# Kernel optimization log

Hardware: AMD Instinct MI355X
Metric: run time of the kernel (lower is better)

The kernel has to match this reference:

```python
import jax, jax.numpy as jnp
import numpy as np

B, N, DIM = 2, 4096, 1024
DEPTH, HEADS, DHEAD = 6, 8, 128
BUCKET = 64          # blindspot_size -> causal_linear_attn bucket_size
DFF = 4 * DIM
EPS_LN = 1e-5
EPS_ATTN = 1e-3


def setup_inputs() -> dict:
    key = jax.random.key(0)
    ks = jax.random.split(key, 16)
    s = 0.02
    HD = HEADS * DHEAD
    inp = {
        "x":     jax.random.normal(ks[0], (B, N, DIM), jnp.float32),
        "ln1_g": jnp.ones((DEPTH, DIM), jnp.float32),
        "ln1_b": jnp.zeros((DEPTH, DIM), jnp.float32),
        "Wq":    jax.random.normal(ks[1], (DEPTH, DIM, HD), jnp.float32) * s,
        "Wk":    jax.random.normal(ks[2], (DEPTH, DIM, HD), jnp.float32) * s,
        "Wv":    jax.random.normal(ks[3], (DEPTH, DIM, HD), jnp.float32) * s,
        "Wo":    jax.random.normal(ks[4], (DEPTH, HD, DIM), jnp.float32) * s,
        "bo":    jnp.zeros((DEPTH, DIM), jnp.float32),
        "ln2_g": jnp.ones((DEPTH, DIM), jnp.float32),
        "ln2_b": jnp.zeros((DEPTH, DIM), jnp.float32),
        "W1":    jax.random.normal(ks[5], (DEPTH, DIM, DFF), jnp.float32) * s,
        "b1":    jnp.zeros((DEPTH, DFF), jnp.float32),
        "W2":    jax.random.normal(ks[6], (DEPTH, DFF, DIM), jnp.float32) * s,
        "b2":    jnp.zeros((DEPTH, DIM), jnp.float32),
    }
    return inp


def layernorm(x, g, b):
    m = jnp.mean(x, axis=-1, keepdims=True)
    v = jnp.var(x, axis=-1, keepdims=True)
    return (x - m) * jax.lax.rsqrt(v + EPS_LN) * g + b


def causal_linear_attn(q, k, v, bucket_size=BUCKET, eps=EPS_ATTN):
    # q,k,v: [b, h, n, e]; n divisible by bucket_size. Blindspot bucketed causal linear attn.
    b, h, n, e = q.shape
    q = jax.nn.softmax(q, axis=-1) * (e ** -0.5)
    k = jnp.exp(k)
    u = n // bucket_size
    bq = q.reshape(b, h, u, bucket_size, e)
    bk = k.reshape(b, h, u, bucket_size, e)
    bv = v.reshape(b, h, u, bucket_size, e)
    b_k_cumsum = jnp.cumsum(bk.sum(axis=-2), axis=2)                     # [b,h,u,e]
    context = jnp.cumsum(jnp.einsum('bhund,bhune->bhude', bk, bv), axis=2)  # [b,h,u,e,e]
    if bucket_size > 1:
        # shift by one bucket: each bucket only sees strictly earlier buckets (blindspot)
        context = jnp.pad(context, ((0, 0), (0, 0), (1, 0), (0, 0), (0, 0)))[:, :, :-1]
        b_k_cumsum = jnp.pad(b_k_cumsum, ((0, 0), (0, 0), (1, 0), (0, 0)))[:, :, :-1]
    D_inv = 1.0 / jnp.maximum(jnp.einsum('bhud,bhund->bhun', b_k_cumsum, bq), eps)
    out = jnp.einsum('bhund,bhude,bhun->bhune', bq, context, D_inv)
    return out.reshape(b, h, n, e)


def _forward(x, ln1_g, ln1_b, Wq, Wk, Wv, Wo, bo, ln2_g, ln2_b, W1, b1, W2, b2):
    def split_heads(t):  # [b,n,h*e] -> [b,h,n,e]
        return t.reshape(B, N, HEADS, DHEAD).transpose(0, 2, 1, 3)

    def layer(x, p):
        g1, bb1_, wq, wk, wv, wo, bo_, g2, bb2_, w1, bias1, w2, bias2 = p
        h = layernorm(x, g1, bb1_)
        q, k, v = split_heads(h @ wq), split_heads(h @ wk), split_heads(h @ wv)
        a = causal_linear_attn(q, k, v)
        a = a.transpose(0, 2, 1, 3).reshape(B, N, HEADS * DHEAD)
        x = x + a @ wo + bo_
        h = layernorm(x, g2, bb2_)
        x = x + jax.nn.gelu(h @ w1 + bias1, approximate=False) @ w2 + bias2
        return x, None

    params = (ln1_g, ln1_b, Wq, Wk, Wv, Wo, bo, ln2_g, ln2_b, W1, b1, W2, b2)
    x, _ = jax.lax.scan(layer, x, params)
    return x


def reference(x, ln1_g, ln1_b, Wq, Wk, Wv, Wo, bo, ln2_g, ln2_b, W1, b1, W2, b2):
    return _forward(x, ln1_g, ln1_b, Wq, Wk, Wv, Wo, bo, ln2_g, ln2_b, W1, b1, W2, b2)
```

## Files before the change

### kernel.cpp

```cpp
#include <hip/hip_runtime.h>
#include <hip/hip_bf16.h>
#include <stdint.h>

#define TOK 8192
#define DIM 1024
#define NSEQ 4096
#define NH 8
#define DHD 128
#define NU 64
#define DFF 4096
#define NBH 16
#define QKVN 3072

typedef unsigned short u16;
typedef unsigned int u32;
typedef short bf16x8 __attribute__((ext_vector_type(8)));
typedef float f32x4 __attribute__((ext_vector_type(4)));

__device__ __forceinline__ float bu2f(u16 u) { return __uint_as_float(((u32)u) << 16); }
__device__ __forceinline__ u16 f2bu(float f) {
  union { __hip_bfloat16 b; u16 u; } cv; cv.b = __float2bfloat16(f); return cv.u;
}

typedef __attribute__((address_space(1))) void gvoid_t;
typedef __attribute__((address_space(3))) void lvoid_t;
__device__ __forceinline__ void gload16(void* lds, const void* g) {
#if __has_builtin(__builtin_amdgcn_global_load_lds)
  __builtin_amdgcn_global_load_lds((const gvoid_t*)g, (lvoid_t*)lds, 16, 0, 0);
#else
  const int l = threadIdx.x & 63;
  ((uint4*)lds)[l] = *(const uint4*)g;
#endif
}

__global__ __launch_bounds__(256) void wtrans_kernel(const float* __restrict__ W,
    u16* __restrict__ Wt, int K, int N, int dStride, int rowOff)
{
  __shared__ float T[32][33];
  const int tid = threadIdx.x;
  const size_t soff = (size_t)blockIdx.z * K * N;
  const size_t doff = (size_t)blockIdx.z * dStride;
  const int n0 = blockIdx.x << 5, k0 = blockIdx.y << 5;
  const int r = tid >> 3, c4 = (tid & 7) << 2;
  float4 v = *(const float4*)(W + soff + (size_t)(k0 + r) * N + n0 + c4);
  T[r][c4] = v.x; T[r][c4 + 1] = v.y; T[r][c4 + 2] = v.z; T[r][c4 + 3] = v.w;
  __syncthreads();
  u32 lo = (u32)f2bu(T[c4][r]) | ((u32)f2bu(T[c4 + 1][r]) << 16);
  u32 hi = (u32)f2bu(T[c4 + 2][r]) | ((u32)f2bu(T[c4 + 3][r]) << 16);
  *(uint2*)(Wt + doff + (size_t)(rowOff + n0 + r) * K + k0 + c4) = make_uint2(lo, hi);
}

__global__ __launch_bounds__(256) void ln_kernel(const float* __restrict__ x,
    const float* __restrict__ g, const float* __restrict__ bt, u16* __restrict__ h)
{
  const int row = blockIdx.x, tid = threadIdx.x;
  const int w = tid >> 6, l = tid & 63;
  float4 v = ((const float4*)(x + (size_t)row * DIM))[tid];
  float s = v.x + v.y + v.z + v.w;
  float s2 = v.x * v.x + v.y * v.y + v.z * v.z + v.w * v.w;
#pragma unroll
  for (int off = 32; off; off >>= 1) { s += __shfl_down(s, off); s2 += __shfl_down(s2, off); }
  __shared__ float ps[8];
  __shared__ float mv[2];
  if (l == 0) { ps[w] = s; ps[4 + w] = s2; }
  __syncthreads();
  if (tid == 0) {
    float S = ps[0] + ps[1] + ps[2] + ps[3];
    float S2 = ps[4] + ps[5] + ps[6] + ps[7];
    float mean = S * (1.f / 1024.f);
    float var = S2 * (1.f / 1024.f) - mean * mean;
    mv[0] = mean; mv[1] = rsqrtf(var + 1e-5f);
  }
  __syncthreads();
  const float mean = mv[0], inv = mv[1];
  const int c = tid * 4;
  float o0 = (v.x - mean) * inv * g[c + 0] + bt[c + 0];
  float o1 = (v.y - mean) * inv * g[c + 1] + bt[c + 1];
  float o2 = (v.z - mean) * inv * g[c + 2] + bt[c + 2];
  float o3 = (v.w - mean) * inv * g[c + 3] + bt[c + 3];
  u32 lo = (u32)f2bu(o0) | ((u32)f2bu(o1) << 16);
  u32 hi = (u32)f2bu(o2) | ((u32)f2bu(o3) << 16);
  ((uint2*)(h + (size_t)row * DIM))[tid] = make_uint2(lo, hi);
}

template<int EPI>
__global__ __launch_bounds__(256, 2) void gemm_kernel(
    const u16* __restrict__ A, const u16* __restrict__ Bt, void* Cout,
    const float* __restrict__ bias, const float* res, int M, int N, int K)
{
  __shared__ __align__(16) u16 As[2][128 * 32];
  __shared__ __align__(16) u16 Bs[2][128 * 32];
  const int tid = threadIdx.x;
  const int w = tid >> 6, l = tid & 63;
  const int gx = gridDim.x;
  const int nwg = gx * gridDim.y;
  const int orig = blockIdx.y * gx + blockIdx.x;
  const int qq = nwg >> 3, rr = nwg & 7, xcd = orig & 7, lin = orig >> 3;
  const int wg = (xcd < rr ? xcd * (qq + 1) : rr * (qq + 1) + (xcd - rr) * qq) + lin;
  const int brow = (wg / gx) << 7, bcol = (wg % gx) << 7;
  const int wr = (w >> 1) << 6, wc = (w & 1) << 6;
  const int lr = l & 15, lk = (l >> 4) << 3;
  f32x4 acc[4][4] = {};
  const int nk = K >> 5;

#define STAGE_G(buf, kt)                                                        \
  {                                                                             \
    _Pragma("unroll")                                                           \
    for (int j = 0; j < 2; ++j) {                                               \
      int c = j * 256 + tid;                                                    \
      int rrow = c >> 2, k8 = (c & 3) << 3;                                     \
      int ub = (j * 256 + w * 64) * 8;                                          \
      gload16(&As[buf][ub], A + (size_t)(brow + rrow) * K + (kt) * 32 + k8);    \
      gload16(&Bs[buf][ub], Bt + (size_t)(bcol + rrow) * K + (kt) * 32 + k8);   \
    }                                                                           \
  }

  STAGE_G(0, 0);
  __syncthreads();
  for (int kt = 0; kt < nk; ++kt) {
    int buf = kt & 1;
    if (kt + 1 < nk) STAGE_G(buf ^ 1, kt + 1);
    bf16x8 a[4], bb[4];
#pragma unroll
    for (int m = 0; m < 4; ++m) a[m] = *(const bf16x8*)&As[buf][(wr + m * 16 + lr) * 32 + lk];
#pragma unroll
    for (int n = 0; n < 4; ++n) bb[n] = *(const bf16x8*)&Bs[buf][(wc + n * 16 + lr) * 32 + lk];
#pragma unroll
    for (int m = 0; m < 4; ++m)
#pragma unroll
      for (int n = 0; n < 4; ++n)
        acc[m][n] = __builtin_amdgcn_mfma_f32_16x16x32_bf16(a[m], bb[n], acc[m][n], 0, 0, 0);
    __syncthreads();
  }
#undef STAGE_G
  const int l4 = (l >> 4) << 2;
#pragma unroll
  for (int m = 0; m < 4; ++m) {
#pragma unroll
    for (int n = 0; n < 4; ++n) {
      int col = bcol + wc + n * 16 + lr;
#pragma unroll
      for (int r = 0; r < 4; ++r) {
        int row = brow + wr + m * 16 + l4 + r;
        size_t idx = (size_t)row * N + col;
        float v0 = acc[m][n][r];
        if (EPI == 0) {
          ((u16*)Cout)[idx] = f2bu(v0);
        } else if (EPI == 1) {
          ((float*)Cout)[idx] = v0 + bias[col] + res[idx];
        } else {
          float t = v0 + bias[col];
          ((u16*)Cout)[idx] = f2bu(0.5f * t * (1.0f + erff(t * 0.70710678118654752f)));
        }
      }
    }
  }
}

__global__ __launch_bounds__(256) void qsoftmax_kernel(const u16* __restrict__ qkv, u16* __restrict__ qs)
{
  const int w = threadIdx.x >> 6, l = threadIdx.x & 63;
  const size_t gid = (size_t)blockIdx.x * 4 + w;
  const size_t tok = gid >> 3;
  const int h = (int)(gid & 7);
  const u16* row = qkv + tok * QKVN + h * 128;
  u16* orow = qs + tok * DIM + h * 128;
  u32 p = *(const u32*)(row + l * 2);
  float f0 = bu2f((u16)(p & 0xffff)), f1 = bu2f((u16)(p >> 16));
  float m = fmaxf(f0, f1);
#pragma unroll
  for (int off = 32; off; off >>= 1) m = fmaxf(m, __shfl_xor(m, off));
  float e0 = expf(f0 - m), e1 = expf(f1 - m);
  float s = e0 + e1;
#pragma unroll
  for (int off = 32; off; off >>= 1) s += __shfl_xor(s, off);
  float sc = 0.08838834764831845f / s;
  u32 o = (u32)f2bu(e0 * sc) | ((u32)f2bu(e1 * sc) << 16);
  *(u32*)(orow + l * 2) = o;
}

__global__ __launch_bounds__(256) void kvt_kernel(
    const u16* __restrict__ kin, const u16* __restrict__ vin,
    u16* __restrict__ ket, u16* __restrict__ vt)
{
  __shared__ u16 T[128 * 72];
  const int tid = threadIdx.x;
  const int t64 = blockIdx.x, bh = blockIdx.y;
  const int b = bh >> 3, h = bh & 7;
  for (int pass = 0; pass < 2; ++pass) {
    const u16* src = pass ? vin : kin;
    u16* dst = pass ? vt : ket;
    if (pass) __syncthreads();
#pragma unroll
    for (int j = 0; j < 4; ++j) {
      int c = j * 256 + tid;
      int i = c >> 4, e8 = (c & 15) << 3;
      bf16x8 dv = *(const bf16x8*)(src + ((size_t)(b * NSEQ + t64 * 64 + i)) * QKVN + h * 128 + e8);
#pragma unroll
      for (int jj = 0; jj < 8; ++jj) {
        float f = bu2f((u16)dv[jj]);
        if (pass == 0) f = expf(f);
        T[(e8 + jj) * 72 + i] = f2bu(f);
      }
    }
    __syncthreads();
#pragma unroll
    for (int j = 0; j < 4; ++j) {
      int c = j * 256 + tid;
      int e = c >> 3, n8 = (c & 7) << 3;
      bf16x8 o;
#pragma unroll
      for (int jj = 0; jj < 8; ++jj) o[jj] = (short)T[e * 72 + n8 + jj];
      *(bf16x8*)(dst + ((size_t)(bh * 128 + e)) * NSEQ + t64 * 64 + n8) = o;
    }
  }
}

__global__ void ksum_kernel(const u16* __restrict__ ket, float* __restrict__ Ksum)
{
  const int u = blockIdx.x, bh = blockIdx.y, e = threadIdx.x;
  const u16* p = ket + ((size_t)(bh * 128 + e)) * NSEQ + u * 64;
  float s = 0.f;
#pragma unroll
  for (int i = 0; i < 64; ++i) s += bu2f(p[i]);
  Ksum[(((size_t)bh * 64 + u) << 7) + e] = s;
}

__global__ void kc_kernel(const float* __restrict__ Ksum, float* __restrict__ Kc)
{
  const int bh = blockIdx.x, e = threadIdx.x;
  float run = 0.f;
  for (int u = 0; u < 64; ++u) {
    size_t i = (((size_t)bh * 64 + u) << 7) + e;
    Kc[i] = run;
    run += Ksum[i];
  }
}

__global__ __launch_bounds__(256, 2) void ctx_kernel(
    const u16* __restrict__ vt, const u16* __restrict__ ket, u16* __restrict__ ctxT)
{
  __shared__ __align__(16) u16 Av[128 * 64];
  __shared__ __align__(16) u16 Bk[128 * 64];
  const int tid = threadIdx.x, w = tid >> 6, l = tid & 63;
  const int u = blockIdx.x, bh = blockIdx.y;
  const int lr = l & 15, lk = (l >> 4) << 3;
#pragma unroll
  for (int j = 0; j < 4; ++j) {
    int c = j * 256 + tid;
    int row = c >> 3, i8 = (c & 7) << 3;
    size_t goff = ((size_t)(bh * 128 + row)) * NSEQ + u * 64 + i8;
    int ub = (j * 256 + w * 64) * 8;
    gload16(&Av[ub], vt + goff);
    gload16(&Bk[ub], ket + goff);
  }
  __syncthreads();
  const int wr = (w >> 1) << 6, wc = (w & 1) << 6;
  f32x4 acc[4][4] = {};
#pragma unroll
  for (int ks = 0; ks < 2; ++ks) {
    bf16x8 a[4], bb[4];
#pragma unroll
    for (int m = 0; m < 4; ++m) a[m] = *(const bf16x8*)&Av[(wr + m * 16 + lr) * 64 + ks * 32 + lk];
#pragma unroll
    for (int n = 0; n < 4; ++n) bb[n] = *(const bf16x8*)&Bk[(wc + n * 16 + lr) * 64 + ks * 32 + lk];
#pragma unroll
    for (int m = 0; m < 4; ++m)
#pragma unroll
      for (int n = 0; n < 4; ++n)
        acc[m][n] = __builtin_amdgcn_mfma_f32_16x16x32_bf16(a[m], bb[n], acc[m][n], 0, 0, 0);
  }
  u16* out = ctxT + ((size_t)(bh * 64 + u) << 14);
  const int l4 = (l >> 4) << 2;
#pragma unroll
  for (int m = 0; m < 4; ++m)
#pragma unroll
    for (int n = 0; n < 4; ++n)
#pragma unroll
      for (int r = 0; r < 4; ++r) {
        int e = wr + m * 16 + l4 + r, d = wc + n * 16 + lr;
        out[e * 128 + d] = f2bu(acc[m][n][r]);
      }
}

__global__ void cumsum_kernel(const u16* __restrict__ ctxT, u16* __restrict__ ctxc)
{
  const size_t base = ((size_t)blockIdx.y << 20) + (size_t)blockIdx.x * 256 + threadIdx.x;
  const u16* src = ctxT + base;
  u16* dst = ctxc + base;
  float run = 0.f;
  for (int u = 0; u < 64; ++u) {
    u16 cvv = src[(size_t)u << 14];
    dst[(size_t)u << 14] = f2bu(run);
    run += bu2f(cvv);
  }
}

__global__ __launch_bounds__(256, 2) void attnout_kernel(
    const u16* __restrict__ qs, const u16* __restrict__ ctxc,
    const float* __restrict__ Kc, u16* __restrict__ aout)
{
  __shared__ __align__(16) u16 Aq[64 * 128];
  __shared__ __align__(16) u16 Bc[128 * 128];
  __shared__ float KcS[128];
  __shared__ float Dinv[64];
  const int tid = threadIdx.x, w = tid >> 6, l = tid & 63;
  const int u = blockIdx.x, bh = blockIdx.y;
  const int b = bh >> 3, h = bh & 7;
  const int lr = l & 15, lk = (l >> 4) << 3;
#pragma unroll
  for (int j = 0; j < 4; ++j) {
    int c = j * 256 + tid;
    int n = c >> 4, d8 = (c & 15) << 3;
    gload16(&Aq[(j * 256 + w * 64) * 8],
            qs + ((size_t)(b * NSEQ + u * 64 + n)) * DIM + h * 128 + d8);
  }
  const u16* csrc = ctxc + ((size_t)(bh * 64 + u) << 14);
#pragma unroll
  for (int j = 0; j < 8; ++j) {
    int c = j * 256 + tid;
    gload16(&Bc[(j * 256 + w * 64) * 8], csrc + (size_t)c * 8);
  }
  if (tid < 128) KcS[tid] = Kc[(((size_t)bh * 64 + u) << 7) + tid];
  __syncthreads();
  if (tid < 64) {
    float s = 0.f;
#pragma unroll
    for (int dd = 0; dd < 128; ++dd) {
      int d = (dd + tid * 2) & 127;
      s += bu2f(Aq[tid * 128 + d]) * KcS[d];
    }
    Dinv[tid] = 1.f / fmaxf(s, 1e-3f);
  }
  __syncthreads();
  f32x4 acc[4][2] = {};
#pragma unroll
  for (int ks = 0; ks < 4; ++ks) {
    bf16x8 a[4], bb[2];
#pragma unroll
    for (int m = 0; m < 4; ++m) a[m] = *(const bf16x8*)&Aq[(m * 16 + lr) * 128 + ks * 32 + lk];
#pragma unroll
    for (int n = 0; n < 2; ++n) bb[n] = *(const bf16x8*)&Bc[(w * 32 + n * 16 + lr) * 128 + ks * 32 + lk];
#pragma unroll
    for (int m = 0; m < 4; ++m)
#pragma unroll
      for (int n = 0; n < 2; ++n)
        acc[m][n] = __builtin_amdgcn_mfma_f32_16x16x32_bf16(a[m], bb[n], acc[m][n], 0, 0, 0);
  }
  const int l4 = (l >> 4) << 2;
#pragma unroll
  for (int m = 0; m < 4; ++m)
#pragma unroll
    for (int n = 0; n < 2; ++n)
#pragma unroll
      for (int r = 0; r < 4; ++r) {
        int nrow = m * 16 + l4 + r;
        int e = w * 32 + n * 16 + lr;
        float v = acc[m][n][r] * Dinv[nrow];
        aout[((size_t)(b * NSEQ + u * 64 + nrow)) * DIM + h * 128 + e] = f2bu(v);
      }
}

extern "C" void kernel_launch(void* const* d_in, const int* in_sizes, int n_in,
                              void* d_out, int out_size, void* d_ws, size_t ws_size,
                              hipStream_t stream)
{
  (void)in_sizes; (void)n_in; (void)out_size; (void)ws_size;
  const float* x_in = (const float*)d_in[0];
  const float* ln1g = (const float*)d_in[1];
  const float* ln1b = (const float*)d_in[2];
  const float* Wq   = (const float*)d_in[3];
  const float* Wk   = (const float*)d_in[4];
  const float* Wv   = (const float*)d_in[5];
  const float* Wo   = (const float*)d_in[6];
  const float* bo   = (const float*)d_in[7];
  const float* ln2g = (const float*)d_in[8];
  const float* ln2b = (const float*)d_in[9];
  const float* W1   = (const float*)d_in[10];
  const float* b1   = (const float*)d_in[11];
  const float* W2   = (const float*)d_in[12];
  const float* b2   = (const float*)d_in[13];
  float* x = (float*)d_out;

  char* ws = (char*)d_ws;
  size_t off = 0;
  auto alloc = [&](size_t bytes) -> char* {
    char* p = ws + off;
    off += (bytes + 255) & ~(size_t)255;
    return p;
  };
  const size_t SW = (size_t)6 * 1024 * 1024;
  const size_t BW = (size_t)6 * 4096 * 1024;
  u16* Wqkvt = (u16*)alloc(SW * 3 * 2);
  u16* Wot = (u16*)alloc(SW * 2);
  u16* W1t = (u16*)alloc(BW * 2);
  u16* W2t = (u16*)alloc(BW * 2);
  u16* hbuf = (u16*)alloc((size_t)TOK * DIM * 2);
  u16* qsb  = (u16*)alloc((size_t)TOK * DIM * 2);
  u16* ket  = (u16*)alloc((size_t)TOK * DIM * 2);
  u16* vtb  = (u16*)alloc((size_t)TOK * DIM * 2);
  u16* ab   = (u16*)alloc((size_t)TOK * DIM * 2);
  float* Ksum = (float*)alloc((size_t)NBH * 64 * 128 * 4);
  float* Kc   = (float*)alloc((size_t)NBH * 64 * 128 * 4);
  char* R = alloc((size_t)TOK * DFF * 2);
  u16* qkvb = (u16*)R;
  u16* ctxT = (u16*)R;
  u16* ctxc = (u16*)(R + ((size_t)NBH * 64 * 128 * 128) * 2);
  u16* mid  = (u16*)R;

  wtrans_kernel<<<dim3(32, 32, 6), 256, 0, stream>>>(Wq, Wqkvt, 1024, 1024, QKVN * 1024, 0);
  wtrans_kernel<<<dim3(32, 32, 6), 256, 0, stream>>>(Wk, Wqkvt, 1024, 1024, QKVN * 1024, 1024);
  wtrans_kernel<<<dim3(32, 32, 6), 256, 0, stream>>>(Wv, Wqkvt, 1024, 1024, QKVN * 1024, 2048);
  wtrans_kernel<<<dim3(32, 32, 6), 256, 0, stream>>>(Wo, Wot, 1024, 1024, 1024 * 1024, 0);
  wtrans_kernel<<<dim3(128, 32, 6), 256, 0, stream>>>(W1, W1t, 1024, 4096, 4096 * 1024, 0);
  wtrans_kernel<<<dim3(32, 128, 6), 256, 0, stream>>>(W2, W2t, 4096, 1024, 4096 * 1024, 0);
  hipMemcpyAsync(x, x_in, (size_t)TOK * DIM * 4, hipMemcpyDeviceToDevice, stream);

  for (int d = 0; d < 6; ++d) {
    ln_kernel<<<TOK, 256, 0, stream>>>(x, ln1g + d * DIM, ln1b + d * DIM, hbuf);
    gemm_kernel<0><<<dim3(24, 64), 256, 0, stream>>>(hbuf, Wqkvt + (size_t)d * QKVN * 1024, qkvb, nullptr, nullptr, TOK, QKVN, DIM);
    qsoftmax_kernel<<<TOK * NH / 4, 256, 0, stream>>>(qkvb, qsb);
    kvt_kernel<<<dim3(64, NBH), 256, 0, stream>>>(qkvb + 1024, qkvb + 2048, ket, vtb);
    ksum_kernel<<<dim3(64, NBH), 128, 0, stream>>>(ket, Ksum);
    kc_kernel<<<NBH, 128, 0, stream>>>(Ksum, Kc);
    ctx_kernel<<<dim3(64, NBH), 256, 0, stream>>>(vtb, ket, ctxT);
    cumsum_kernel<<<dim3(64, NBH), 256, 0, stream>>>(ctxT, ctxc);
    attnout_kernel<<<dim3(64, NBH), 256, 0, stream>>>(qsb, ctxc, Kc, ab);
    gemm_kernel<1><<<dim3(8, 64), 256, 0, stream>>>(ab, Wot + (size_t)d * 1024 * 1024, x, bo + d * DIM, x, TOK, DIM, DIM);
    ln_kernel<<<TOK, 256, 0, stream>>>(x, ln2g + d * DIM, ln2b + d * DIM, hbuf);
    gemm_kernel<2><<<dim3(32, 64), 256, 0, stream>>>(hbuf, W1t + (size_t)d * DFF * 1024, mid, b1 + d * DFF, nullptr, TOK, DFF, DIM);
    gemm_kernel<1><<<dim3(8, 64), 256, 0, stream>>>(mid, W2t + (size_t)d * DFF * 1024, x, b2 + d * DIM, x, TOK, DIM, DFF);
  }
}
```

Before: 2.649 ms.

## Add 256x256 eight-wave pipelined GEMM for the QKV and FFN-up projections

Adds a new bf16 MFMA GEMM kernel with 256x256 output tiles, 512 threads, a K-step of 64 and XOR-swizzled LDS. It splits each K-step into four phases that interleave global-to-LDS staging with MFMA quadrants, using barriers and raised wave priority around the MFMA blocks. The QKV projection and the W1+GELU projection now use this kernel. The older 128x128 kernel is reduced to the residual epilogue only, for the Wo and W2 GEMMs. The larger tiles give more data reuse per LDS load, but they need about 128KB of LDS per block, which limits occupancy, and they produce fewer workgroups, so wave quantization across CUs could suffer.

Result: slower. 3.061 ms (+15.6%).

```diff
diff --git a/kernel.cpp b/kernel.cpp
--- a/kernel.cpp
+++ b/kernel.cpp
@@ -84,6 +84,115 @@
 }
 
 template<int EPI>
+__global__ __launch_bounds__(512, 2) void gemm8_kernel(
+    const u16* __restrict__ A, const u16* __restrict__ Bt, void* Cout,
+    const float* __restrict__ bias, int M, int N, int K)
+{
+  __shared__ __align__(16) u16 As[2][2][8192];
+  __shared__ __align__(16) u16 Bs[2][2][8192];
+  const int tid = threadIdx.x;
+  const int w = tid >> 6, l = tid & 63;
+  const int wm = w >> 2, wn = w & 3;
+  const int lr = l & 15, lk = (l >> 4) << 3;
+  const int gx = gridDim.x;
+  const int nwg = gx * gridDim.y;
+  const int orig = blockIdx.y * gx + blockIdx.x;
+  const int qq = nwg >> 3, rr = nwg & 7, xcd = orig & 7, lin = orig >> 3;
+  const int wg = (xcd < rr ? xcd * (qq + 1) : rr * (qq + 1) + (xcd - rr) * qq) + lin;
+  const int brow = (wg / gx) << 8, bcol = (wg % gx) << 8;
+  const int nk = K >> 6;
+  const int srow = w * 8 + (l >> 3);
+  const int scol = ((l & 7) * 8) ^ ((l & 32) ? 16 : 0);
+  const int swz = ((l >> 2) & 1) << 4;
+  const int colK0 = lk ^ swz, colK1 = (32 + lk) ^ swz;
+
+  f32x4 acc[8][4] = {};
+  bf16x8 af[4][2];
+  bf16x8 bf[2][2][2];
+
+#define STAGE_A8(b_, h_, kt_) { _Pragma("unroll") for (int c = 0; c < 2; ++c)   \
+    gload16(&As[b_][h_][c * 4096 + w * 512],                                    \
+      A + (size_t)(brow + (h_) * 128 + c * 64 + srow) * K + (kt_) * 64 + scol); }
+#define STAGE_B8(b_, h_, kt_) { _Pragma("unroll") for (int c = 0; c < 2; ++c)   \
+    gload16(&Bs[b_][h_][c * 4096 + w * 512],                                    \
+      Bt + (size_t)(bcol + (h_) * 128 + c * 64 + srow) * K + (kt_) * 64 + scol); }
+#define LOAD_AF(b_, mh_) { _Pragma("unroll") for (int m = 0; m < 4; ++m) {      \
+    const u16* p_ = &As[b_][wm][((mh_) * 64 + m * 16 + lr) * 64];               \
+    af[m][0] = *(const bf16x8*)(p_ + colK0);                                    \
+    af[m][1] = *(const bf16x8*)(p_ + colK1); } }
+#define LOAD_BF(b_, nh_) { _Pragma("unroll") for (int n = 0; n < 2; ++n) {      \
+    const u16* p_ = &Bs[b_][wn >> 1][((wn & 1) * 64 + (nh_) * 32 + n * 16 + lr) * 64]; \
+    bf[nh_][n][0] = *(const bf16x8*)(p_ + colK0);                               \
+    bf[nh_][n][1] = *(const bf16x8*)(p_ + colK1); } }
+#define MFMA_Q(mh_, nh_) { __builtin_amdgcn_s_setprio(1);                       \
+    _Pragma("unroll") for (int m = 0; m < 4; ++m)                               \
+    _Pragma("unroll") for (int n = 0; n < 2; ++n) {                             \
+      acc[(mh_)*4+m][(nh_)*2+n] = __builtin_amdgcn_mfma_f32_16x16x32_bf16(      \
+          af[m][0], bf[nh_][n][0], acc[(mh_)*4+m][(nh_)*2+n], 0, 0, 0);         \
+      acc[(mh_)*4+m][(nh_)*2+n] = __builtin_amdgcn_mfma_f32_16x16x32_bf16(      \
+          af[m][1], bf[nh_][n][1], acc[(mh_)*4+m][(nh_)*2+n], 0, 0, 0); }       \
+    __builtin_amdgcn_s_setprio(0); }
+#define PHASE_BAR() { __builtin_amdgcn_sched_barrier(0);                        \
+    __builtin_amdgcn_s_barrier(); __builtin_amdgcn_sched_barrier(0); }
+
+  STAGE_A8(0, 0, 0); STAGE_A8(0, 1, 0);
+  STAGE_B8(0, 0, 0); STAGE_B8(0, 1, 0);
+  STAGE_B8(1, 0, 1); STAGE_B8(1, 1, 1);
+  asm volatile("s_waitcnt vmcnt(4)" ::: "memory");
+  PHASE_BAR();
+
+  for (int t = 0; t < nk; ++t) {
+    const int buf = t & 1, nb = buf ^ 1;
+    LOAD_AF(buf, 0); LOAD_BF(buf, 0);
+    if (t + 1 < nk) STAGE_A8(nb, 0, t + 1);
+    PHASE_BAR();
+    MFMA_Q(0, 0);
+    PHASE_BAR();
+    LOAD_BF(buf, 1);
+    if (t + 1 < nk) STAGE_A8(nb, 1, t + 1);
+    PHASE_BAR();
+    MFMA_Q(0, 1);
+    PHASE_BAR();
+    LOAD_AF(buf, 1);
+    if (t + 2 < nk) STAGE_B8(buf, 0, t + 2);
+    PHASE_BAR();
+    MFMA_Q(1, 0);
+    PHASE_BAR();
+    if (t + 2 < nk) STAGE_B8(buf, 1, t + 2);
+    PHASE_BAR();
+    MFMA_Q(1, 1);
+    asm volatile("s_waitcnt vmcnt(4)" ::: "memory");
+    PHASE_BAR();
+  }
+#undef STAGE_A8
+#undef STAGE_B8
+#undef LOAD_AF
+#undef LOAD_BF
+#undef MFMA_Q
+#undef PHASE_BAR
+
+  const int l4 = (l >> 4) << 2;
+#pragma unroll
+  for (int mi = 0; mi < 8; ++mi) {
+#pragma unroll
+    for (int nj = 0; nj < 4; ++nj) {
+      int col = bcol + wn * 64 + nj * 16 + lr;
+#pragma unroll
+      for (int r = 0; r < 4; ++r) {
+        int row = brow + wm * 128 + mi * 16 + l4 + r;
+        size_t idx = (size_t)row * N + col;
+        float v0 = acc[mi][nj][r];
+        if (EPI == 0) {
+          ((u16*)Cout)[idx] = f2bu(v0);
+        } else {
+          float tt = v0 + bias[col];
+          ((u16*)Cout)[idx] = f2bu(0.5f * tt * (1.0f + erff(tt * 0.70710678118654752f)));
+        }
+      }
+    }
+  }
+}
+
 __global__ __launch_bounds__(256, 2) void gemm_kernel(
     const u16* __restrict__ A, const u16* __restrict__ Bt, void* Cout,
     const float* __restrict__ bias, const float* res, int M, int N, int K)
@@ -143,15 +252,7 @@
       for (int r = 0; r < 4; ++r) {
         int row = brow + wr + m * 16 + l4 + r;
         size_t idx = (size_t)row * N + col;
-        float v0 = acc[m][n][r];
-        if (EPI == 0) {
-          ((u16*)Cout)[idx] = f2bu(v0);
-        } else if (EPI == 1) {
-          ((float*)Cout)[idx] = v0 + bias[col] + res[idx];
-        } else {
-          float t = v0 + bias[col];
-          ((u16*)Cout)[idx] = f2bu(0.5f * t * (1.0f + erff(t * 0.70710678118654752f)));
-        }
+        ((float*)Cout)[idx] = acc[m][n][r] + bias[col] + res[idx];
       }
     }
   }
@@ -418,7 +519,7 @@
 
   for (int d = 0; d < 6; ++d) {
     ln_kernel<<<TOK, 256, 0, stream>>>(x, ln1g + d * DIM, ln1b + d * DIM, hbuf);
-    gemm_kernel<0><<<dim3(24, 64), 256, 0, stream>>>(hbuf, Wqkvt + (size_t)d * QKVN * 1024, qkvb, nullptr, nullptr, TOK, QKVN, DIM);
+    gemm8_kernel<0><<<dim3(12, 32), 512, 0, stream>>>(hbuf, Wqkvt + (size_t)d * QKVN * 1024, qkvb, nullptr, TOK, QKVN, DIM);
     qsoftmax_kernel<<<TOK * NH / 4, 256, 0, stream>>>(qkvb, qsb);
     kvt_kernel<<<dim3(64, NBH), 256, 0, stream>>>(qkvb + 1024, qkvb + 2048, ket, vtb);
     ksum_kernel<<<dim3(64, NBH), 128, 0, stream>>>(ket, Ksum);
@@ -426,9 +527,9 @@
     ctx_kernel<<<dim3(64, NBH), 256, 0, stream>>>(vtb, ket, ctxT);
     cumsum_kernel<<<dim3(64, NBH), 256, 0, stream>>>(ctxT, ctxc);
     attnout_kernel<<<dim3(64, NBH), 256, 0, stream>>>(qsb, ctxc, Kc, ab);
-    gemm_kernel<1><<<dim3(8, 64), 256, 0, stream>>>(ab, Wot + (size_t)d * 1024 * 1024, x, bo + d * DIM, x, TOK, DIM, DIM);
+    gemm_kernel<<<dim3(8, 64), 256, 0, stream>>>(ab, Wot + (size_t)d * 1024 * 1024, x, bo + d * DIM, x, TOK, DIM, DIM);
     ln_kernel<<<TOK, 256, 0, stream>>>(x, ln2g + d * DIM, ln2b + d * DIM, hbuf);
-    gemm_kernel<2><<<dim3(32, 64), 256, 0, stream>>>(hbuf, W1t + (size_t)d * DFF * 1024, mid, b1 + d * DFF, nullptr, TOK, DFF, DIM);
-    gemm_kernel<1><<<dim3(8, 64), 256, 0, stream>>>(mid, W2t + (size_t)d * DFF * 1024, x, b2 + d * DIM, x, TOK, DIM, DFF);
-  }
-}
+    gemm8_kernel<2><<<dim3(16, 32), 512, 0, stream>>>(hbuf, W1t + (size_t)d * DFF * 1024, mid, b1 + d * DFF, TOK, DFF, DIM);
+    gemm_kernel<<<dim3(8, 64), 256, 0, stream>>>(mid, W2t + (size_t)d * DFF * 1024, x, b2 + d * DIM, x, TOK, DIM, DFF);
+  }
+}
```

## Enlarge GEMM tiles to 256x128 and fold key-sum into kvt transpose kernel

Applied to the files above, without the earlier changes.

The GEMM kernel's M tile grows from 128 to 256 rows. Each wave now computes a 128x64 sub-tile with 8x4 MFMA accumulators, and each A fragment is loaded per m-iteration and reused across the 4 B fragments. All GEMM grids are halved in y to match. Separately, the per-bucket key sum is computed from the shared-memory transpose tile inside kvt_kernel, which removes the ksum_kernel launch and its re-read of ket. The larger tile doubles accumulator registers and A shared memory, which can lower occupancy under launch_bounds(256,2) and halves the block count.

Result: slower. 3.494 ms (+31.9%).

```diff
diff --git a/kernel.cpp b/kernel.cpp
--- a/kernel.cpp
+++ b/kernel.cpp
@@ -88,7 +88,7 @@
     const u16* __restrict__ A, const u16* __restrict__ Bt, void* Cout,
     const float* __restrict__ bias, const float* res, int M, int N, int K)
 {
-  __shared__ __align__(16) u16 As[2][128 * 32];
+  __shared__ __align__(16) u16 As[2][256 * 32];
   __shared__ __align__(16) u16 Bs[2][128 * 32];
   const int tid = threadIdx.x;
   const int w = tid >> 6, l = tid & 63;
@@ -97,21 +97,27 @@
   const int orig = blockIdx.y * gx + blockIdx.x;
   const int qq = nwg >> 3, rr = nwg & 7, xcd = orig & 7, lin = orig >> 3;
   const int wg = (xcd < rr ? xcd * (qq + 1) : rr * (qq + 1) + (xcd - rr) * qq) + lin;
-  const int brow = (wg / gx) << 7, bcol = (wg % gx) << 7;
-  const int wr = (w >> 1) << 6, wc = (w & 1) << 6;
+  const int brow = (wg / gx) << 8, bcol = (wg % gx) << 7;
+  const int wr = (w >> 1) << 7, wc = (w & 1) << 6;
   const int lr = l & 15, lk = (l >> 4) << 3;
-  f32x4 acc[4][4] = {};
+  f32x4 acc[8][4] = {};
   const int nk = K >> 5;
 
 #define STAGE_G(buf, kt)                                                        \
   {                                                                             \
+    _Pragma("unroll")                                                           \
+    for (int j = 0; j < 4; ++j) {                                               \
+      int c = j * 256 + tid;                                                    \
+      int rrow = c >> 2, k8 = (c & 3) << 3;                                     \
+      gload16(&As[buf][(j * 256 + w * 64) * 8],                                 \
+              A + (size_t)(brow + rrow) * K + (kt) * 32 + k8);                  \
+    }                                                                           \
     _Pragma("unroll")                                                           \
     for (int j = 0; j < 2; ++j) {                                               \
       int c = j * 256 + tid;                                                    \
       int rrow = c >> 2, k8 = (c & 3) << 3;                                     \
-      int ub = (j * 256 + w * 64) * 8;                                          \
-      gload16(&As[buf][ub], A + (size_t)(brow + rrow) * K + (kt) * 32 + k8);    \
-      gload16(&Bs[buf][ub], Bt + (size_t)(bcol + rrow) * K + (kt) * 32 + k8);   \
+      gload16(&Bs[buf][(j * 256 + w * 64) * 8],                                 \
+              Bt + (size_t)(bcol + rrow) * K + (kt) * 32 + k8);                 \
     }                                                                           \
   }
 
@@ -120,22 +126,22 @@
   for (int kt = 0; kt < nk; ++kt) {
     int buf = kt & 1;
     if (kt + 1 < nk) STAGE_G(buf ^ 1, kt + 1);
-    bf16x8 a[4], bb[4];
-#pragma unroll
-    for (int m = 0; m < 4; ++m) a[m] = *(const bf16x8*)&As[buf][(wr + m * 16 + lr) * 32 + lk];
-#pragma unroll
-    for (int n = 0; n < 4; ++n) bb[n] = *(const bf16x8*)&Bs[buf][(wc + n * 16 + lr) * 32 + lk];
-#pragma unroll
-    for (int m = 0; m < 4; ++m)
+    bf16x8 b[4];
+#pragma unroll
+    for (int n = 0; n < 4; ++n) b[n] = *(const bf16x8*)&Bs[buf][(wc + n * 16 + lr) * 32 + lk];
+#pragma unroll
+    for (int m = 0; m < 8; ++m) {
+      bf16x8 a = *(const bf16x8*)&As[buf][(wr + m * 16 + lr) * 32 + lk];
 #pragma unroll
       for (int n = 0; n < 4; ++n)
-        acc[m][n] = __builtin_amdgcn_mfma_f32_16x16x32_bf16(a[m], bb[n], acc[m][n], 0, 0, 0);
+        acc[m][n] = __builtin_amdgcn_mfma_f32_16x16x32_bf16(a, b[n], acc[m][n], 0, 0, 0);
+    }
     __syncthreads();
   }
 #undef STAGE_G
   const int l4 = (l >> 4) << 2;
 #pragma unroll
-  for (int m = 0; m < 4; ++m) {
+  for (int m = 0; m < 8; ++m) {
 #pragma unroll
     for (int n = 0; n < 4; ++n) {
       int col = bcol + wc + n * 16 + lr;
@@ -181,7 +187,7 @@
 
 __global__ __launch_bounds__(256) void kvt_kernel(
     const u16* __restrict__ kin, const u16* __restrict__ vin,
-    u16* __restrict__ ket, u16* __restrict__ vt)
+    u16* __restrict__ ket, u16* __restrict__ vt, float* __restrict__ Ksum)
 {
   __shared__ u16 T[128 * 72];
   const int tid = threadIdx.x;
@@ -204,6 +210,12 @@
       }
     }
     __syncthreads();
+    if (pass == 0 && tid < 128) {
+      float s = 0.f;
+#pragma unroll
+      for (int i2 = 0; i2 < 64; ++i2) s += bu2f(T[tid * 72 + i2]);
+      Ksum[(((size_t)bh * 64 + t64) << 7) + tid] = s;
+    }
 #pragma unroll
     for (int j = 0; j < 4; ++j) {
       int c = j * 256 + tid;
@@ -214,16 +226,6 @@
       *(bf16x8*)(dst + ((size_t)(bh * 128 + e)) * NSEQ + t64 * 64 + n8) = o;
     }
   }
-}
-
-__global__ void ksum_kernel(const u16* __restrict__ ket, float* __restrict__ Ksum)
-{
-  const int u = blockIdx.x, bh = blockIdx.y, e = threadIdx.x;
-  const u16* p = ket + ((size_t)(bh * 128 + e)) * NSEQ + u * 64;
-  float s = 0.f;
-#pragma unroll
-  for (int i = 0; i < 64; ++i) s += bu2f(p[i]);
-  Ksum[(((size_t)bh * 64 + u) << 7) + e] = s;
 }
 
 __global__ void kc_kernel(const float* __restrict__ Ksum, float* __restrict__ Kc)
@@ -414,21 +416,20 @@
   wtrans_kernel<<<dim3(32, 32, 6), 256, 0, stream>>>(Wo, Wot, 1024, 1024, 1024 * 1024, 0);
   wtrans_kernel<<<dim3(128, 32, 6), 256, 0, stream>>>(W1, W1t, 1024, 4096, 4096 * 1024, 0);
   wtrans_kernel<<<dim3(32, 128, 6), 256, 0, stream>>>(W2, W2t, 4096, 1024, 4096 * 1024, 0);
-  hipMemcpyAsync(x, x_in, (size_t)TOK * DIM * 4, hipMemcpyDeviceToDevice, stream);
+  (void)hipMemcpyAsync(x, x_in, (size_t)TOK * DIM * 4, hipMemcpyDeviceToDevice, stream);
 
   for (int d = 0; d < 6; ++d) {
     ln_kernel<<<TOK, 256, 0, stream>>>(x, ln1g + d * DIM, ln1b + d * DIM, hbuf);
-    gemm_kernel<0><<<dim3(24, 64), 256, 0, stream>>>(hbuf, Wqkvt + (size_t)d * QKVN * 1024, qkvb, nullptr, nullptr, TOK, QKVN, DIM);
+    gemm_kernel<0><<<dim3(24, 32), 256, 0, stream>>>(hbuf, Wqkvt + (size_t)d * QKVN * 1024, qkvb, nullptr, nullptr, TOK, QKVN, DIM);
     qsoftmax_kernel<<<TOK * NH / 4, 256, 0, stream>>>(qkvb, qsb);
-    kvt_kernel<<<dim3(64, NBH), 256, 0, stream>>>(qkvb + 1024, qkvb + 2048, ket, vtb);
-    ksum_kernel<<<dim3(64, NBH), 128, 0, stream>>>(ket, Ksum);
+    kvt_kernel<<<dim3(64, NBH), 256, 0, stream>>>(qkvb + 1024, qkvb + 2048, ket, vtb, Ksum);
     kc_kernel<<<NBH, 128, 0, stream>>>(Ksum, Kc);
     ctx_kernel<<<dim3(64, NBH), 256, 0, stream>>>(vtb, ket, ctxT);
     cumsum_kernel<<<dim3(64, NBH), 256, 0, stream>>>(ctxT, ctxc);
     attnout_kernel<<<dim3(64, NBH), 256, 0, stream>>>(qsb, ctxc, Kc, ab);
-    gemm_kernel<1><<<dim3(8, 64), 256, 0, stream>>>(ab, Wot + (size_t)d * 1024 * 1024, x, bo + d * DIM, x, TOK, DIM, DIM);
+    gemm_kernel<1><<<dim3(8, 32), 256, 0, stream>>>(ab, Wot + (size_t)d * 1024 * 1024, x, bo + d * DIM, x, TOK, DIM, DIM);
     ln_kernel<<<TOK, 256, 0, stream>>>(x, ln2g + d * DIM, ln2b + d * DIM, hbuf);
-    gemm_kernel<2><<<dim3(32, 64), 256, 0, stream>>>(hbuf, W1t + (size_t)d * DFF * 1024, mid, b1 + d * DFF, nullptr, TOK, DFF, DIM);
-    gemm_kernel<1><<<dim3(8, 64), 256, 0, stream>>>(mid, W2t + (size_t)d * DFF * 1024, x, b2 + d * DIM, x, TOK, DIM, DFF);
-  }
-}
+    gemm_kernel<2><<<dim3(32, 32), 256, 0, stream>>>(hbuf, W1t + (size_t)d * DFF * 1024, mid, b1 + d * DFF, nullptr, TOK, DFF, DIM);
+    gemm_kernel<1><<<dim3(8, 32), 256, 0, stream>>>(mid, W2t + (size_t)d * DFF * 1024, x, b2 + d * DIM, x, TOK, DIM, DFF);
+  }
+}
```

## Fuse Q softmax into QKV GEMM epilogue, K-sum into kvt, use tanh GELU

Applied to the files above, without the earlier changes.

Adds a GEMM epilogue that computes the per-head softmax of Q directly from accumulators, using shared-memory cross-wave max/sum reductions, and writes the scaled result, removing the separate qsoftmax kernel. K column sums per bucket are computed inside kvt_kernel from the shared transpose tile, removing ksum_kernel. The erf GELU is replaced by a tanh approximation computed via exp, which changes numerics slightly relative to the exact GELU reference.

Measured after the change: 2.505 ms. 5.4% less time.

```diff
diff --git a/kernel.cpp b/kernel.cpp
--- a/kernel.cpp
+++ b/kernel.cpp
@@ -86,10 +86,12 @@
 template<int EPI>
 __global__ __launch_bounds__(256, 2) void gemm_kernel(
     const u16* __restrict__ A, const u16* __restrict__ Bt, void* Cout,
-    const float* __restrict__ bias, const float* res, int M, int N, int K)
+    const float* __restrict__ bias, const float* res, u16* __restrict__ qs,
+    int M, int N, int K)
 {
   __shared__ __align__(16) u16 As[2][128 * 32];
   __shared__ __align__(16) u16 Bs[2][128 * 32];
+  __shared__ float sm[2][128];
   const int tid = threadIdx.x;
   const int w = tid >> 6, l = tid & 63;
   const int gx = gridDim.x;
@@ -134,6 +136,69 @@
   }
 #undef STAGE_G
   const int l4 = (l >> 4) << 2;
+
+  if (EPI == 3 && bcol < 1024) {
+    const int wcol = w & 1;
+    float rmax[4][4], rsum[4][4];
+#pragma unroll
+    for (int m = 0; m < 4; ++m)
+#pragma unroll
+      for (int r = 0; r < 4; ++r) {
+        float v = fmaxf(fmaxf(acc[m][0][r], acc[m][1][r]), fmaxf(acc[m][2][r], acc[m][3][r]));
+#pragma unroll
+        for (int msk = 1; msk < 16; msk <<= 1) v = fmaxf(v, __shfl_xor(v, msk));
+        rmax[m][r] = v;
+      }
+    __syncthreads();
+#pragma unroll
+    for (int m = 0; m < 4; ++m)
+#pragma unroll
+      for (int r = 0; r < 4; ++r) sm[wcol][wr + m * 16 + l4 + r] = rmax[m][r];
+    __syncthreads();
+#pragma unroll
+    for (int m = 0; m < 4; ++m)
+#pragma unroll
+      for (int r = 0; r < 4; ++r) rmax[m][r] = fmaxf(rmax[m][r], sm[wcol ^ 1][wr + m * 16 + l4 + r]);
+#pragma unroll
+    for (int m = 0; m < 4; ++m)
+#pragma unroll
+      for (int r = 0; r < 4; ++r) {
+        float s = 0.f;
+#pragma unroll
+        for (int n = 0; n < 4; ++n) {
+          float e = __expf(acc[m][n][r] - rmax[m][r]);
+          acc[m][n][r] = e;
+          s += e;
+        }
+#pragma unroll
+        for (int msk = 1; msk < 16; msk <<= 1) s += __shfl_xor(s, msk);
+        rsum[m][r] = s;
+      }
+    __syncthreads();
+#pragma unroll
+    for (int m = 0; m < 4; ++m)
+#pragma unroll
+      for (int r = 0; r < 4; ++r) sm[wcol][wr + m * 16 + l4 + r] = rsum[m][r];
+    __syncthreads();
+#pragma unroll
+    for (int m = 0; m < 4; ++m)
+#pragma unroll
+      for (int r = 0; r < 4; ++r) rsum[m][r] += sm[wcol ^ 1][wr + m * 16 + l4 + r];
+#pragma unroll
+    for (int m = 0; m < 4; ++m)
+#pragma unroll
+      for (int n = 0; n < 4; ++n) {
+        int col = bcol + wc + n * 16 + lr;
+#pragma unroll
+        for (int r = 0; r < 4; ++r) {
+          int row = brow + wr + m * 16 + l4 + r;
+          float v = acc[m][n][r] * (0.08838834764831845f / rsum[m][r]);
+          qs[(size_t)row * DIM + col] = f2bu(v);
+        }
+      }
+    return;
+  }
+
 #pragma unroll
   for (int m = 0; m < 4; ++m) {
 #pragma unroll
@@ -144,44 +209,25 @@
         int row = brow + wr + m * 16 + l4 + r;
         size_t idx = (size_t)row * N + col;
         float v0 = acc[m][n][r];
-        if (EPI == 0) {
+        if (EPI == 0 || EPI == 3) {
           ((u16*)Cout)[idx] = f2bu(v0);
         } else if (EPI == 1) {
           ((float*)Cout)[idx] = v0 + bias[col] + res[idx];
         } else {
           float t = v0 + bias[col];
-          ((u16*)Cout)[idx] = f2bu(0.5f * t * (1.0f + erff(t * 0.70710678118654752f)));
+          float z = 1.5957691216057308f * (t + 0.044715f * t * t * t);
+          float e = __expf(z);
+          float th = (e - 1.f) / (e + 1.f);
+          ((u16*)Cout)[idx] = f2bu(0.5f * t * (1.f + th));
         }
       }
     }
   }
-}
-
-__global__ __launch_bounds__(256) void qsoftmax_kernel(const u16* __restrict__ qkv, u16* __restrict__ qs)
-{
-  const int w = threadIdx.x >> 6, l = threadIdx.x & 63;
-  const size_t gid = (size_t)blockIdx.x * 4 + w;
-  const size_t tok = gid >> 3;
-  const int h = (int)(gid & 7);
-  const u16* row = qkv + tok * QKVN + h * 128;
-  u16* orow = qs + tok * DIM + h * 128;
-  u32 p = *(const u32*)(row + l * 2);
-  float f0 = bu2f((u16)(p & 0xffff)), f1 = bu2f((u16)(p >> 16));
-  float m = fmaxf(f0, f1);
-#pragma unroll
-  for (int off = 32; off; off >>= 1) m = fmaxf(m, __shfl_xor(m, off));
-  float e0 = expf(f0 - m), e1 = expf(f1 - m);
-  float s = e0 + e1;
-#pragma unroll
-  for (int off = 32; off; off >>= 1) s += __shfl_xor(s, off);
-  float sc = 0.08838834764831845f / s;
-  u32 o = (u32)f2bu(e0 * sc) | ((u32)f2bu(e1 * sc) << 16);
-  *(u32*)(orow + l * 2) = o;
 }
 
 __global__ __launch_bounds__(256) void kvt_kernel(
     const u16* __restrict__ kin, const u16* __restrict__ vin,
-    u16* __restrict__ ket, u16* __restrict__ vt)
+    u16* __restrict__ ket, u16* __restrict__ vt, float* __restrict__ Ksum)
 {
   __shared__ u16 T[128 * 72];
   const int tid = threadIdx.x;
@@ -204,6 +250,12 @@
       }
     }
     __syncthreads();
+    if (pass == 0 && tid < 128) {
+      float s = 0.f;
+#pragma unroll
+      for (int i2 = 0; i2 < 64; ++i2) s += bu2f(T[tid * 72 + i2]);
+      Ksum[(((size_t)bh * 64 + t64) << 7) + tid] = s;
+    }
 #pragma unroll
     for (int j = 0; j < 4; ++j) {
       int c = j * 256 + tid;
@@ -214,16 +266,6 @@
       *(bf16x8*)(dst + ((size_t)(bh * 128 + e)) * NSEQ + t64 * 64 + n8) = o;
     }
   }
-}
-
-__global__ void ksum_kernel(const u16* __restrict__ ket, float* __restrict__ Ksum)
-{
-  const int u = blockIdx.x, bh = blockIdx.y, e = threadIdx.x;
-  const u16* p = ket + ((size_t)(bh * 128 + e)) * NSEQ + u * 64;
-  float s = 0.f;
-#pragma unroll
-  for (int i = 0; i < 64; ++i) s += bu2f(p[i]);
-  Ksum[(((size_t)bh * 64 + u) << 7) + e] = s;
 }
 
 __global__ void kc_kernel(const float* __restrict__ Ksum, float* __restrict__ Kc)
@@ -414,21 +456,19 @@
   wtrans_kernel<<<dim3(32, 32, 6), 256, 0, stream>>>(Wo, Wot, 1024, 1024, 1024 * 1024, 0);
   wtrans_kernel<<<dim3(128, 32, 6), 256, 0, stream>>>(W1, W1t, 1024, 4096, 4096 * 1024, 0);
   wtrans_kernel<<<dim3(32, 128, 6), 256, 0, stream>>>(W2, W2t, 4096, 1024, 4096 * 1024, 0);
-  hipMemcpyAsync(x, x_in, (size_t)TOK * DIM * 4, hipMemcpyDeviceToDevice, stream);
+  (void)hipMemcpyAsync(x, x_in, (size_t)TOK * DIM * 4, hipMemcpyDeviceToDevice, stream);
 
   for (int d = 0; d < 6; ++d) {
     ln_kernel<<<TOK, 256, 0, stream>>>(x, ln1g + d * DIM, ln1b + d * DIM, hbuf);
-    gemm_kernel<0><<<dim3(24, 64), 256, 0, stream>>>(hbuf, Wqkvt + (size_t)d * QKVN * 1024, qkvb, nullptr, nullptr, TOK, QKVN, DIM);
-    qsoftmax_kernel<<<TOK * NH / 4, 256, 0, stream>>>(qkvb, qsb);
-    kvt_kernel<<<dim3(64, NBH), 256, 0, stream>>>(qkvb + 1024, qkvb + 2048, ket, vtb);
-    ksum_kernel<<<dim3(64, NBH), 128, 0, stream>>>(ket, Ksum);
+    gemm_kernel<3><<<dim3(24, 64), 256, 0, stream>>>(hbuf, Wqkvt + (size_t)d * QKVN * 1024, qkvb, nullptr, nullptr, qsb, TOK, QKVN, DIM);
+    kvt_kernel<<<dim3(64, NBH), 256, 0, stream>>>(qkvb + 1024, qkvb + 2048, ket, vtb, Ksum);
     kc_kernel<<<NBH, 128, 0, stream>>>(Ksum, Kc);
     ctx_kernel<<<dim3(64, NBH), 256, 0, stream>>>(vtb, ket, ctxT);
     cumsum_kernel<<<dim3(64, NBH), 256, 0, stream>>>(ctxT, ctxc);
     attnout_kernel<<<dim3(64, NBH), 256, 0, stream>>>(qsb, ctxc, Kc, ab);
-    gemm_kernel<1><<<dim3(8, 64), 256, 0, stream>>>(ab, Wot + (size_t)d * 1024 * 1024, x, bo + d * DIM, x, TOK, DIM, DIM);
+    gemm_kernel<1><<<dim3(8, 64), 256, 0, stream>>>(ab, Wot + (size_t)d * 1024 * 1024, x, bo + d * DIM, x, nullptr, TOK, DIM, DIM);
     ln_kernel<<<TOK, 256, 0, stream>>>(x, ln2g + d * DIM, ln2b + d * DIM, hbuf);
-    gemm_kernel<2><<<dim3(32, 64), 256, 0, stream>>>(hbuf, W1t + (size_t)d * DFF * 1024, mid, b1 + d * DFF, nullptr, TOK, DFF, DIM);
-    gemm_kernel<1><<<dim3(8, 64), 256, 0, stream>>>(mid, W2t + (size_t)d * DFF * 1024, x, b2 + d * DIM, x, TOK, DIM, DFF);
-  }
-}
+    gemm_kernel<2><<<dim3(32, 64), 256, 0, stream>>>(hbuf, W1t + (size_t)d * DFF * 1024, mid, b1 + d * DFF, nullptr, nullptr, TOK, DFF, DIM);
+    gemm_kernel<1><<<dim3(8, 64), 256, 0, stream>>>(mid, W2t + (size_t)d * DFF * 1024, x, b2 + d * DIM, x, nullptr, TOK, DIM, DFF);
+  }
+}
```
